# Performance work log

Hardware: AMD Instinct MI355X
Metric: run time of the kernel (lower is better)

## Reference

```python
import jax, jax.numpy as jnp
import numpy as np

B, N, E, T, DIN, H, G, ND, NT, L = 4, 10000, 320000, 16, 16, 64, 64, 16, 3, 7


def _mlp2(x, W1, b1, W2, b2):
    # Linear -> LeakyReLU -> (Dropout: eval identity) -> Linear -> LeakyReLU
    h = jax.nn.leaky_relu(x @ W1 + b1)
    return jax.nn.leaky_relu(h @ W2 + b2)


def _gcn_conv(x, src, dst, ew, nt, W1, b1, W2, b2):
    # x: [B,N,D], nt: [B,N,ND], ew: [*,E,1] broadcastable over batch
    x_in = _mlp2(jnp.concatenate([x, nt], axis=-1), W1, b1, W2, b2)  # [B,N,G]
    msgs = x_in[:, src, :] * ew                                      # gather + weight, [B,E,G]
    aggr = jnp.zeros(x_in.shape, x_in.dtype).at[:, dst, :].add(msgs) # scatter-add, [B,N,G]
    return x + aggr


def _gru(x, Wx, Wh, bx, bh):
    # PyTorch-style GRU over time axis. x: [B,N,T,DIN] -> hs: [T,B,N,H]
    xw = jnp.einsum('bntd,dh->tbnh', x, Wx) + bx  # precompute input projections [T,B,N,3H]
    h0 = jnp.zeros(x.shape[:2] + (Wh.shape[0],), x.dtype)

    def step(h, xw_t):
        hw = h @ Wh + bh
        xr, xz, xn = jnp.split(xw_t, 3, axis=-1)
        hr, hz, hn = jnp.split(hw, 3, axis=-1)
        r = jax.nn.sigmoid(xr + hr)
        z = jax.nn.sigmoid(xz + hz)
        n = jnp.tanh(xn + r * hn)
        h_new = (1 - z) * n + z * h
        return h_new, h_new

    _, hs = jax.lax.scan(step, h0, xw)
    return hs


def reference(input_day, edge_attr, gru_Wx, gru_Wh, gru_bx, gru_bh,
              rnn_fc_W, rnn_fc_b,
              e_emb, e_c0_W1, e_c0_b1, e_c0_W2, e_c0_b2,
              e_c1_W1, e_c1_b1, e_c1_W2, e_c1_b2,
              e_fm_W1, e_fm_b1, e_fm_W2, e_fm_b2,
              g_emb, g_c0_W1, g_c0_b1, g_c0_W2, g_c0_b2,
              g_c1_W1, g_c1_b1, g_c1_W2, g_c1_b2,
              gcn_fc_W, gcn_fc_b,
              edge_index, node_type_ids):
    src, dst = edge_index[0], edge_index[1]

    # KRNN encoder (GRU) + max over time + FC head
    hs = _gru(input_day, gru_Wx, gru_Wh, gru_bx, gru_bh)  # [T,B,N,H]
    rnn_out = hs.max(axis=0)                              # kr_out.max(dim=-2) -> [B,N,H]
    y_rnn = rnn_out @ rnn_fc_W + rnn_fc_b                 # [B,N,L]

    # EdgeNet: GCN stack on static edge_attr, then per-edge pair MLP -> gate
    nt_e = jnp.broadcast_to(e_emb[node_type_ids][None], (B, N, ND))
    ew0 = edge_attr.reshape(1, E, 1)
    x = rnn_out
    x = _gcn_conv(x, src, dst, ew0, nt_e, e_c0_W1, e_c0_b1, e_c0_W2, e_c0_b2)
    x = _gcn_conv(x, src, dst, ew0, nt_e, e_c1_W1, e_c1_b1, e_c1_W2, e_c1_b2)
    edge_x = jnp.concatenate([x[:, src, :], x[:, dst, :]], axis=-1)  # [B,E,2G]
    h = jax.nn.leaky_relu(edge_x @ e_fm_W1 + e_fm_b1)
    edge_gate = jax.nn.relu(h @ e_fm_W2 + e_fm_b2)                   # [B,E,1]

    # Main GCNNet with learned edge gates
    nt_g = jnp.broadcast_to(g_emb[node_type_ids][None], (B, N, ND))
    x = rnn_out
    x = _gcn_conv(x, src, dst, edge_gate, nt_g, g_c0_W1, g_c0_b1, g_c0_W2, g_c0_b2)
    x = _gcn_conv(x, src, dst, edge_gate, nt_g, g_c1_W1, g_c1_b1, g_c1_W2, g_c1_b2)
    y_gcn = x @ gcn_fc_W + gcn_fc_b                                  # [B,N,L]

    return y_rnn + y_gcn


def setup_inputs() -> dict:
    key = jax.random.key(0)
    ks = iter(jax.random.split(key, 48))

    def nrm(shape, s=0.1):
        return jax.random.normal(next(ks), shape, jnp.float32) * s

    inp = {}
    inp['input_day'] = jax.random.normal(next(ks), (B, N, T, DIN), jnp.float32)
    inp['edge_index'] = jax.random.randint(next(ks), (2, E), 0, N)
    inp['node_type_ids'] = jax.random.randint(next(ks), (N,), 0, NT)
    inp['edge_attr'] = jax.random.uniform(next(ks), (E,), jnp.float32)

    inp['gru_Wx'] = nrm((DIN, 3 * H))
    inp['gru_Wh'] = nrm((H, 3 * H))
    inp['gru_bx'] = jnp.zeros((3 * H,), jnp.float32)
    inp['gru_bh'] = jnp.zeros((3 * H,), jnp.float32)
    inp['rnn_fc_W'] = nrm((H, L))
    inp['rnn_fc_b'] = jnp.zeros((L,), jnp.float32)

    inp['e_emb'] = nrm((NT, ND))
    inp['g_emb'] = nrm((NT, ND))
    for pre, in_dim in (('e_c0', H + ND), ('e_c1', G + ND), ('g_c0', H + ND), ('g_c1', G + ND)):
        inp[pre + '_W1'] = nrm((in_dim, G))
        inp[pre + '_b1'] = jnp.zeros((G,), jnp.float32)
        inp[pre + '_W2'] = nrm((G, G))
        inp[pre + '_b2'] = jnp.zeros((G,), jnp.float32)

    inp['e_fm_W1'] = nrm((2 * G, G))
    inp['e_fm_b1'] = jnp.zeros((G,), jnp.float32)
    inp['e_fm_W2'] = nrm((G, 1))
    inp['e_fm_b2'] = jnp.zeros((1,), jnp.float32)

    inp['gcn_fc_W'] = nrm((G, L))
    inp['gcn_fc_b'] = jnp.zeros((L,), jnp.float32)
    return inp
```

## Files before the change

### kernel.cpp

```cpp
#include <hip/hip_runtime.h>
#include <hip/hip_bf16.h>

#define NB 4
#define NN 10000
#define NE 320000
#define BN 40000
#define NL 7

typedef float f32x4 __attribute__((ext_vector_type(4)));
typedef __bf16 bf16x8 __attribute__((ext_vector_type(8)));

__device__ __forceinline__ float bf2f(unsigned short u){
  unsigned x = ((unsigned)u) << 16;
  return __builtin_bit_cast(float, x);
}
__device__ __forceinline__ unsigned short f2bf(float f){
  unsigned u = __builtin_bit_cast(unsigned, f);
  u += 0x7fffu + ((u >> 16) & 1u);
  return (unsigned short)(u >> 16);
}
__device__ __forceinline__ __bf16 f2b(float f){
  return __builtin_bit_cast(__bf16, f2bf(f));
}
__device__ __forceinline__ bf16x8 zero8(){
  uint4 z = make_uint4(0u,0u,0u,0u);
  return __builtin_bit_cast(bf16x8, z);
}
__device__ __forceinline__ bf16x8 ld8bf(const unsigned short* p){
  uint4 u = *(const uint4*)p;
  return __builtin_bit_cast(bf16x8, u);
}
__device__ __forceinline__ bf16x8 ld8f(const float* p){
  float4 a = *(const float4*)p;
  float4 b = *(const float4*)(p+4);
  bf16x8 r;
  r[0]=f2b(a.x); r[1]=f2b(a.y); r[2]=f2b(a.z); r[3]=f2b(a.w);
  r[4]=f2b(b.x); r[5]=f2b(b.y); r[6]=f2b(b.z); r[7]=f2b(b.w);
  return r;
}
__device__ __forceinline__ float frcp(float x){ return __builtin_amdgcn_rcpf(x); }
__device__ __forceinline__ float sigm(float x){ return frcp(1.f+__expf(-x)); }
__device__ __forceinline__ float tanh_(float x){ return 1.f - 2.f*frcp(__expf(2.f*x)+1.f); }
__device__ __forceinline__ float lrelu(float x){ return x > 0.f ? x : 0.01f*x; }

#define LDS_WAIT() asm volatile("s_waitcnt lgkmcnt(0)" ::: "memory")

__global__ __launch_bounds__(256, 2) void gru_kernel(
    const float* __restrict__ xd,
    const float* __restrict__ Wx,
    const float* __restrict__ Wh,
    const float* __restrict__ bx,
    const float* __restrict__ bh,
    float* __restrict__ rnn)
{
  __shared__ __attribute__((aligned(16))) unsigned short WhT[192][72];
  __shared__ __attribute__((aligned(16))) unsigned short WxT[192][40];
  __shared__ __attribute__((aligned(16))) unsigned short hb[4][16][72];
  int tid = threadIdx.x;
  int wave = tid >> 6, lane = tid & 63;
  int ln16 = lane & 15, quad = lane >> 4;

  for (int i = tid; i < 64*192; i += 256){
    int k = i / 192, n = i - k*192;
    WhT[n][k] = f2bf(Wh[i]);
  }
  for (int i = tid; i < 16*192; i += 256){
    int k = i / 192, n = i - k*192;
    WxT[n][k] = f2bf(Wx[i]);
    WxT[n][16+k] = 0;
  }
  for (int i = tid; i < 4*16*72; i += 256) ((unsigned short*)hb)[i] = 0;
  __syncthreads();

  int rowbase = blockIdx.x * 64 + wave * 16;

  bf16x8 whf[2][12];
  #pragma unroll
  for (int kt=0; kt<2; ++kt)
    #pragma unroll
    for (int nt=0; nt<12; ++nt)
      whf[kt][nt] = ld8bf(&WhT[nt*16 + ln16][kt*32 + quad*8]);

  float br_[4], bz_[4], bxn_[4], bhn_[4];
  #pragma unroll
  for (int j=0;j<4;++j){
    br_[j]  = bx[j*16+ln16]     + bh[j*16+ln16];
    bz_[j]  = bx[(4+j)*16+ln16] + bh[(4+j)*16+ln16];
    bxn_[j] = bx[(8+j)*16+ln16];
    bhn_[j] = bh[(8+j)*16+ln16];
  }

  f32x4 hprev[4], vmax[4];
  #pragma unroll
  for (int j=0;j<4;++j){
    hprev[j] = (f32x4){0.f,0.f,0.f,0.f};
    vmax[j]  = (f32x4){-1e30f,-1e30f,-1e30f,-1e30f};
  }

  const float* xrow = xd + (size_t)(rowbase + ln16) * 256;
  unsigned short* hrow = &hb[wave][ln16][0];

  bf16x8 axc = (quad < 2) ? ld8f(xrow + quad*8) : zero8();

  for (int t = 0; t < 16; ++t){
    bf16x8 axn = (t < 15 && quad < 2) ? ld8f(xrow + (t+1)*16 + quad*8) : zero8();
    bf16x8 ah0 = ld8bf(hrow + quad*8);
    bf16x8 ah1 = ld8bf(hrow + 32 + quad*8);

    #pragma unroll
    for (int j=0;j<4;++j){
      bf16x8 xr = ld8bf(&WxT[j*16+ln16][quad*8]);
      bf16x8 xz = ld8bf(&WxT[(4+j)*16+ln16][quad*8]);
      bf16x8 xn = ld8bf(&WxT[(8+j)*16+ln16][quad*8]);
      f32x4 ar = (f32x4){br_[j],br_[j],br_[j],br_[j]};
      ar = __builtin_amdgcn_mfma_f32_16x16x32_bf16(axc, xr, ar, 0,0,0);
      ar = __builtin_amdgcn_mfma_f32_16x16x32_bf16(ah0, whf[0][j], ar, 0,0,0);
      ar = __builtin_amdgcn_mfma_f32_16x16x32_bf16(ah1, whf[1][j], ar, 0,0,0);
      f32x4 az = (f32x4){bz_[j],bz_[j],bz_[j],bz_[j]};
      az = __builtin_amdgcn_mfma_f32_16x16x32_bf16(axc, xz, az, 0,0,0);
      az = __builtin_amdgcn_mfma_f32_16x16x32_bf16(ah0, whf[0][4+j], az, 0,0,0);
      az = __builtin_amdgcn_mfma_f32_16x16x32_bf16(ah1, whf[1][4+j], az, 0,0,0);
      f32x4 an = (f32x4){bxn_[j],bxn_[j],bxn_[j],bxn_[j]};
      an = __builtin_amdgcn_mfma_f32_16x16x32_bf16(axc, xn, an, 0,0,0);
      f32x4 ah = (f32x4){bhn_[j],bhn_[j],bhn_[j],bhn_[j]};
      ah = __builtin_amdgcn_mfma_f32_16x16x32_bf16(ah0, whf[0][8+j], ah, 0,0,0);
      ah = __builtin_amdgcn_mfma_f32_16x16x32_bf16(ah1, whf[1][8+j], ah, 0,0,0);
      #pragma unroll
      for (int i=0;i<4;++i){
        float r  = sigm(ar[i]);
        float z  = sigm(az[i]);
        float nn = tanh_(an[i] + r * ah[i]);
        float h  = fmaf(z, hprev[j][i]-nn, nn);
        hprev[j][i] = h;
        vmax[j][i] = fmaxf(vmax[j][i], h);
        hb[wave][quad*4+i][j*16+ln16] = f2bf(h);
      }
    }
    LDS_WAIT();
    axc = axn;
  }
  #pragma unroll
  for (int j=0;j<4;++j)
    #pragma unroll
    for (int i=0;i<4;++i)
      rnn[(size_t)(rowbase + quad*4 + i)*64 + j*16 + ln16] = vmax[j][i];
}

__global__ __launch_bounds__(256, 2) void mlp2_kernel(
    const float* __restrict__ x,
    const int* __restrict__ ntid,
    const float* __restrict__ emb,
    const float* __restrict__ W1,
    const float* __restrict__ b1,
    const float* __restrict__ W2,
    const float* __restrict__ b2,
    unsigned short* __restrict__ out)
{
  __shared__ __attribute__((aligned(16))) unsigned short W1T[64][96];
  __shared__ __attribute__((aligned(16))) unsigned short W2T[64][72];
  __shared__ __attribute__((aligned(16))) unsigned short hb[4][16][72];
  __shared__ float sb1[64], sb2[64];
  int tid = threadIdx.x;
  for (int i=tid;i<80*64;i+=256){ int k=i>>6, n=i&63; W1T[n][k]=f2bf(W1[i]); }
  for (int i=tid;i<64*16;i+=256){ int n=i>>4, k=80+(i&15); W1T[n][k]=0; }
  for (int i=tid;i<64*64;i+=256){ int k=i>>6, n=i&63; W2T[n][k]=f2bf(W2[i]); }
  if (tid<64){ sb1[tid]=b1[tid]; sb2[tid]=b2[tid]; }
  __syncthreads();

  int wave = tid>>6, lane = tid&63, ln16 = lane&15, quad = lane>>4;
  int row0 = blockIdx.x*64 + wave*16;
  int r_ = row0 + ln16;
  const float* xr = x + (size_t)r_*64;
  bf16x8 a0 = ld8f(xr + quad*8);
  bf16x8 a1 = ld8f(xr + 32 + quad*8);
  int id = ntid[r_ % NN];
  bf16x8 a2 = (quad<2) ? ld8f(emb + id*16 + quad*8) : zero8();

  f32x4 acc[4];
  #pragma unroll
  for (int nt=0;nt<4;++nt){
    float bb = sb1[nt*16+ln16];
    acc[nt] = (f32x4){bb,bb,bb,bb};
    acc[nt] = __builtin_amdgcn_mfma_f32_16x16x32_bf16(a0, ld8bf(&W1T[nt*16+ln16][quad*8]),    acc[nt], 0,0,0);
    acc[nt] = __builtin_amdgcn_mfma_f32_16x16x32_bf16(a1, ld8bf(&W1T[nt*16+ln16][32+quad*8]), acc[nt], 0,0,0);
    acc[nt] = __builtin_amdgcn_mfma_f32_16x16x32_bf16(a2, ld8bf(&W1T[nt*16+ln16][64+quad*8]), acc[nt], 0,0,0);
  }
  #pragma unroll
  for (int nt=0;nt<4;++nt)
    #pragma unroll
    for (int i=0;i<4;++i)
      hb[wave][quad*4+i][nt*16+ln16] = f2bf(lrelu(acc[nt][i]));
  LDS_WAIT();
  bf16x8 h0 = ld8bf(&hb[wave][ln16][quad*8]);
  bf16x8 h1 = ld8bf(&hb[wave][ln16][32+quad*8]);
  f32x4 acc2[4];
  #pragma unroll
  for (int nt=0;nt<4;++nt){
    float bb = sb2[nt*16+ln16];
    acc2[nt] = (f32x4){bb,bb,bb,bb};
    acc2[nt] = __builtin_amdgcn_mfma_f32_16x16x32_bf16(h0, ld8bf(&W2T[nt*16+ln16][quad*8]),    acc2[nt], 0,0,0);
    acc2[nt] = __builtin_amdgcn_mfma_f32_16x16x32_bf16(h1, ld8bf(&W2T[nt*16+ln16][32+quad*8]), acc2[nt], 0,0,0);
  }
  #pragma unroll
  for (int nt=0;nt<4;++nt)
    #pragma unroll
    for (int i=0;i<4;++i)
      out[(size_t)(row0+quad*4+i)*64 + nt*16+ln16] = f2bf(lrelu(acc2[nt][i]));
}

__global__ __launch_bounds__(256, 2) void uv_kernel(
    const float* __restrict__ x,
    const float* __restrict__ W1,
    unsigned short* __restrict__ uvp)
{
  __shared__ __attribute__((aligned(16))) unsigned short WT[128][72];
  int tid=threadIdx.x;
  for (int i=tid;i<64*64;i+=256){
    int k=i>>6, n=i&63;
    WT[n][k]    = f2bf(W1[i]);
    WT[64+n][k] = f2bf(W1[64*64 + i]);
  }
  __syncthreads();
  int wave=tid>>6, lane=tid&63, ln16=lane&15, quad=lane>>4;
  int row0 = blockIdx.x*64 + wave*16;
  const float* xr = x + (size_t)(row0+ln16)*64;
  bf16x8 a0 = ld8f(xr + quad*8);
  bf16x8 a1 = ld8f(xr + 32 + quad*8);
  f32x4 acc[8];
  #pragma unroll
  for (int nt=0;nt<8;++nt){
    acc[nt] = (f32x4){0.f,0.f,0.f,0.f};
    acc[nt] = __builtin_amdgcn_mfma_f32_16x16x32_bf16(a0, ld8bf(&WT[nt*16+ln16][quad*8]),    acc[nt], 0,0,0);
    acc[nt] = __builtin_amdgcn_mfma_f32_16x16x32_bf16(a1, ld8bf(&WT[nt*16+ln16][32+quad*8]), acc[nt], 0,0,0);
  }
  #pragma unroll
  for (int nt=0;nt<8;++nt)
    #pragma unroll
    for (int i=0;i<4;++i)
      uvp[(size_t)(row0+quad*4+i)*128 + nt*16+ln16] = f2bf(acc[nt][i]);
}

__global__ __launch_bounds__(256) void count_kernel(const int* __restrict__ ei, int* __restrict__ counts){
  int e = blockIdx.x*256+threadIdx.x;
  atomicAdd(&counts[ei[NE+e]], 1);
}
__global__ __launch_bounds__(1024) void scan_kernel(const int* __restrict__ counts,
                                                    int* __restrict__ rowptr, int* __restrict__ cursor){
  __shared__ int incl[10240];
  __shared__ int wsum[16];
  int tid=threadIdx.x, wave=tid>>6, lane=tid&63;
  int base = wave*640;
  int carry=0;
  #pragma unroll
  for (int c=0;c<10;++c){
    int i = base + c*64 + lane;
    int v = (i<NN)? counts[i] : 0;
    int s = v;
    #pragma unroll
    for (int off=1;off<64;off<<=1){
      int t_ = __shfl_up(s, off);
      if (lane>=off) s += t_;
    }
    s += carry;
    incl[base + c*64 + lane] = s;
    carry = __shfl(s, 63);
  }
  if (lane==63) wsum[wave]=carry;
  __syncthreads();
  if (wave==0){
    int w_ = (lane<16)? wsum[lane]:0;
    #pragma unroll
    for (int off=1;off<16;off<<=1){
      int t_ = __shfl_up(w_, off);
      if (lane>=off) w_ += t_;
    }
    if (lane<16) wsum[lane]=w_;
  }
  __syncthreads();
  int woff = (wave>0)? wsum[wave-1] : 0;
  #pragma unroll
  for (int c=0;c<10;++c){
    int i = base + c*64 + lane;
    if (i<NN){
      int excl = incl[i] + woff - counts[i];
      rowptr[i]=excl; cursor[i]=excl;
    }
  }
  if (tid==0) rowptr[NN]=wsum[15];
}
__global__ __launch_bounds__(256) void fill_kernel(const int* __restrict__ ei,
                                                   const float* __restrict__ ea,
                                                   int* __restrict__ cursor,
                                                   int* __restrict__ ssrc,
                                                   float* __restrict__ wcsr){
  int e = blockIdx.x*256+threadIdx.x;
  int d = ei[NE+e];
  int pos = atomicAdd(&cursor[d],1);
  ssrc[pos]=ei[e];
  wcsr[pos]=ea[e];
}

__global__ __launch_bounds__(256) void aggr_kernel(
    const float* x,
    const unsigned short* __restrict__ xin,
    const int* __restrict__ rowptr,
    const int* __restrict__ ssrc,
    const float* __restrict__ wp,
    int bstride,
    float* out)
{
  int tid=threadIdx.x;
  int wave=tid>>6, lane=tid&63;
  int sub=lane>>4, l=lane&15;
  int bid = blockIdx.x*4 + wave;
  int b = bid / NN, n = bid - b*NN;
  int p0 = rowptr[n], p1 = rowptr[n+1];
  const unsigned short* xb_ = xin + (size_t)b*NN*64;
  const float* wb = wp + (size_t)b*bstride;
  float a0=0.f, a1=0.f, a2=0.f, a3=0.f;
  #pragma unroll 4
  for (int p=p0+sub; p<p1; p+=4){
    int s = ssrc[p];
    float w = wb[p];
    uint2 m = *(const uint2*)(xb_ + (size_t)s*64 + l*4);
    a0 += bf2f((unsigned short)(m.x & 0xffffu)) * w;
    a1 += bf2f((unsigned short)(m.x >> 16)) * w;
    a2 += bf2f((unsigned short)(m.y & 0xffffu)) * w;
    a3 += bf2f((unsigned short)(m.y >> 16)) * w;
  }
  a0 += __shfl_xor(a0,16); a0 += __shfl_xor(a0,32);
  a1 += __shfl_xor(a1,16); a1 += __shfl_xor(a1,32);
  a2 += __shfl_xor(a2,16); a2 += __shfl_xor(a2,32);
  a3 += __shfl_xor(a3,16); a3 += __shfl_xor(a3,32);
  if (sub==0){
    float4 base = *(const float4*)(x + (size_t)bid*64 + l*4);
    float4 o; o.x=base.x+a0; o.y=base.y+a1; o.z=base.z+a2; o.w=base.w+a3;
    *(float4*)(out + (size_t)bid*64 + l*4) = o;
  }
}

__global__ __launch_bounds__(256) void aggr_final_kernel(
    const float* x,
    const unsigned short* __restrict__ xin,
    const int* __restrict__ rowptr,
    const int* __restrict__ ssrc,
    const float* __restrict__ wp,
    const float* __restrict__ rnn,
    const float* __restrict__ Wr, const float* __restrict__ br,
    const float* __restrict__ Wg, const float* __restrict__ bg,
    float* __restrict__ out)
{
  __shared__ float sWr[448], sWg[448], sb[7];
  int tid=threadIdx.x;
  for (int i=tid;i<448;i+=256){ sWr[i]=Wr[i]; sWg[i]=Wg[i]; }
  if (tid<7) sb[tid]=br[tid]+bg[tid];
  __syncthreads();
  int wave=tid>>6, lane=tid&63;
  int sub=lane>>4, l=lane&15;
  int bid = blockIdx.x*4 + wave;
  int b = bid / NN, n = bid - b*NN;
  int p0 = rowptr[n], p1 = rowptr[n+1];
  const unsigned short* xb_ = xin + (size_t)b*NN*64;
  const float* wb = wp + (size_t)b*NE;
  float a0=0.f, a1=0.f, a2=0.f, a3=0.f;
  #pragma unroll 4
  for (int p=p0+sub; p<p1; p+=4){
    int s = ssrc[p];
    float w = wb[p];
    uint2 m = *(const uint2*)(xb_ + (size_t)s*64 + l*4);
    a0 += bf2f((unsigned short)(m.x & 0xffffu)) * w;
    a1 += bf2f((unsigned short)(m.x >> 16)) * w;
    a2 += bf2f((unsigned short)(m.y & 0xffffu)) * w;
    a3 += bf2f((unsigned short)(m.y >> 16)) * w;
  }
  a0 += __shfl_xor(a0,16); a0 += __shfl_xor(a0,32);
  a1 += __shfl_xor(a1,16); a1 += __shfl_xor(a1,32);
  a2 += __shfl_xor(a2,16); a2 += __shfl_xor(a2,32);
  a3 += __shfl_xor(a3,16); a3 += __shfl_xor(a3,32);
  if (sub==0){
    float4 base = *(const float4*)(x + (size_t)bid*64 + l*4);
    float o0=base.x+a0, o1=base.y+a1, o2=base.z+a2, o3=base.w+a3;
    float4 rr = *(const float4*)(rnn + (size_t)bid*64 + l*4);
    float part[7];
    #pragma unroll
    for (int q=0;q<7;++q)
      part[q] = o0*sWg[(l*4+0)*7+q] + o1*sWg[(l*4+1)*7+q]
              + o2*sWg[(l*4+2)*7+q] + o3*sWg[(l*4+3)*7+q]
              + rr.x*sWr[(l*4+0)*7+q] + rr.y*sWr[(l*4+1)*7+q]
              + rr.z*sWr[(l*4+2)*7+q] + rr.w*sWr[(l*4+3)*7+q];
    #pragma unroll
    for (int q=0;q<7;++q){
      part[q] += __shfl_xor(part[q],1);
      part[q] += __shfl_xor(part[q],2);
      part[q] += __shfl_xor(part[q],4);
      part[q] += __shfl_xor(part[q],8);
    }
    if (l==0){
      #pragma unroll
      for (int q=0;q<7;++q) out[(size_t)bid*7+q] = part[q] + sb[q];
    }
  }
}

__global__ __launch_bounds__(256) void gate_kernel(
    const unsigned short* __restrict__ uvp,
    const int* __restrict__ rowptr,
    const int* __restrict__ ssrc,
    const float* __restrict__ b1,
    const float* __restrict__ W2,
    const float* __restrict__ b2,
    float* __restrict__ gate)
{
  int tid=threadIdx.x;
  int wave=tid>>6, lane=tid&63;
  int sub=lane>>4, l=lane&15;
  int bid = blockIdx.x*4 + wave;
  int b = bid / NN, n = bid - b*NN;
  int p0 = rowptr[n], p1 = rowptr[n+1];
  const unsigned short* ub = uvp + (size_t)b*NN*128;
  uint2 vu = *(const uint2*)(ub + (size_t)n*128 + 64 + l*4);
  float v0=bf2f((unsigned short)(vu.x&0xffffu)), v1=bf2f((unsigned short)(vu.x>>16));
  float v2=bf2f((unsigned short)(vu.y&0xffffu)), v3=bf2f((unsigned short)(vu.y>>16));
  float4 bb = *(const float4*)(b1 + l*4);
  float4 ww = *(const float4*)(W2 + l*4);
  float b2v = b2[0];
  float* gb = gate + (size_t)b*NE;
  #pragma unroll 4
  for (int p=p0+sub; p<p1; p+=4){
    int s = ssrc[p];
    uint2 uu = *(const uint2*)(ub + (size_t)s*128 + l*4);
    float h0 = lrelu(bf2f((unsigned short)(uu.x&0xffffu)) + v0 + bb.x);
    float h1 = lrelu(bf2f((unsigned short)(uu.x>>16))     + v1 + bb.y);
    float h2 = lrelu(bf2f((unsigned short)(uu.y&0xffffu)) + v2 + bb.z);
    float h3 = lrelu(bf2f((unsigned short)(uu.y>>16))     + v3 + bb.w);
    float part = h0*ww.x + h1*ww.y + h2*ww.z + h3*ww.w;
    part += __shfl_xor(part,1);
    part += __shfl_xor(part,2);
    part += __shfl_xor(part,4);
    part += __shfl_xor(part,8);
    if (l==0){
      float g = part + b2v;
      gb[p] = g>0.f ? g : 0.f;
    }
  }
}

extern "C" void kernel_launch(void* const* d_in, const int* in_sizes, int n_in,
                              void* d_out, int out_size, void* d_ws, size_t ws_size,
                              hipStream_t stream)
{
  (void)in_sizes; (void)n_in; (void)out_size; (void)ws_size;
  const float* input_day = (const float*)d_in[0];
  const int* ei    = (const int*)d_in[1];
  const int* ntid  = (const int*)d_in[2];
  const float* edge_attr = (const float*)d_in[3];
  const float* gWx = (const float*)d_in[4];
  const float* gWh = (const float*)d_in[5];
  const float* gbx = (const float*)d_in[6];
  const float* gbh = (const float*)d_in[7];
  const float* rW  = (const float*)d_in[8];
  const float* rb  = (const float*)d_in[9];
  const float* eemb= (const float*)d_in[10];
  const float* gemb= (const float*)d_in[11];
  const float* ec0W1=(const float*)d_in[12];
  const float* ec0b1=(const float*)d_in[13];
  const float* ec0W2=(const float*)d_in[14];
  const float* ec0b2=(const float*)d_in[15];
  const float* ec1W1=(const float*)d_in[16];
  const float* ec1b1=(const float*)d_in[17];
  const float* ec1W2=(const float*)d_in[18];
  const float* ec1b2=(const float*)d_in[19];
  const float* gc0W1=(const float*)d_in[20];
  const float* gc0b1=(const float*)d_in[21];
  const float* gc0W2=(const float*)d_in[22];
  const float* gc0b2=(const float*)d_in[23];
  const float* gc1W1=(const float*)d_in[24];
  const float* gc1b1=(const float*)d_in[25];
  const float* gc1W2=(const float*)d_in[26];
  const float* gc1b2=(const float*)d_in[27];
  const float* efmW1=(const float*)d_in[28];
  const float* efmb1=(const float*)d_in[29];
  const float* efmW2=(const float*)d_in[30];
  const float* efmb2=(const float*)d_in[31];
  const float* gcnW =(const float*)d_in[32];
  const float* gcnb =(const float*)d_in[33];

  char* ws = (char*)d_ws;
  float*          rnn = (float*)(ws);
  float*          xe  = (float*)(ws + 10240000);
  unsigned short* xin = (unsigned short*)(ws + 20480000);
  unsigned short* uvp = (unsigned short*)(ws + 25600000);
  float*          gat = (float*)(ws + 35840000);
  int* rowptr= (int*)(ws + 40960000);
  int* cursor= (int*)(ws + 41000064);
  int* counts= (int*)(ws + 41040064);
  int*   ssrc= (int*)(ws + 41080064);
  float* wcsr= (float*)(ws + 42360064);

  hipMemsetAsync(counts, 0, NN*sizeof(int), stream);
  count_kernel<<<NE/256, 256, 0, stream>>>(ei, counts);
  scan_kernel<<<1, 1024, 0, stream>>>(counts, rowptr, cursor);
  fill_kernel<<<NE/256, 256, 0, stream>>>(ei, edge_attr, cursor, ssrc, wcsr);

  gru_kernel<<<625, 256, 0, stream>>>(input_day, gWx, gWh, gbx, gbh, rnn);

  mlp2_kernel<<<625, 256, 0, stream>>>(rnn, ntid, eemb, ec0W1, ec0b1, ec0W2, ec0b2, xin);
  aggr_kernel<<<BN/4, 256, 0, stream>>>(rnn, xin, rowptr, ssrc, wcsr, 0, xe);
  mlp2_kernel<<<625, 256, 0, stream>>>(xe, ntid, eemb, ec1W1, ec1b1, ec1W2, ec1b2, xin);
  aggr_kernel<<<BN/4, 256, 0, stream>>>(xe, xin, rowptr, ssrc, wcsr, 0, xe);

  uv_kernel<<<625, 256, 0, stream>>>(xe, efmW1, uvp);
  gate_kernel<<<BN/4, 256, 0, stream>>>(uvp, rowptr, ssrc, efmb1, efmW2, efmb2, gat);

  mlp2_kernel<<<625, 256, 0, stream>>>(rnn, ntid, gemb, gc0W1, gc0b1, gc0W2, gc0b2, xin);
  aggr_kernel<<<BN/4, 256, 0, stream>>>(rnn, xin, rowptr, ssrc, gat, NE, xe);
  mlp2_kernel<<<625, 256, 0, stream>>>(xe, ntid, gemb, gc1W1, gc1b1, gc1W2, gc1b2, xin);
  aggr_final_kernel<<<BN/4, 256, 0, stream>>>(xe, xin, rowptr, ssrc, gat, rnn,
                                              rW, rb, gcnW, gcnb, (float*)d_out);
}
```

Before: 470.1 us.

## Transpose GRU MFMA operands, fold biases into the matmul, pack bf16 stores

```diff
diff --git a/kernel.cpp b/kernel.cpp
--- a/kernel.cpp
+++ b/kernel.cpp
@@ -26,17 +26,24 @@
   uint4 z = make_uint4(0u,0u,0u,0u);
   return __builtin_bit_cast(bf16x8, z);
 }
+__device__ __forceinline__ bf16x8 one8(){
+  uint4 z = make_uint4(0x3f80u,0u,0u,0u);
+  return __builtin_bit_cast(bf16x8, z);
+}
 __device__ __forceinline__ bf16x8 ld8bf(const unsigned short* p){
   uint4 u = *(const uint4*)p;
   return __builtin_bit_cast(bf16x8, u);
 }
+__device__ __forceinline__ unsigned pk2(float lo, float hi){
+  unsigned r;
+  asm("v_cvt_pk_bf16_f32 %0, %1, %2" : "=v"(r) : "v"(lo), "v"(hi));
+  return r;
+}
 __device__ __forceinline__ bf16x8 ld8f(const float* p){
   float4 a = *(const float4*)p;
   float4 b = *(const float4*)(p+4);
-  bf16x8 r;
-  r[0]=f2b(a.x); r[1]=f2b(a.y); r[2]=f2b(a.z); r[3]=f2b(a.w);
-  r[4]=f2b(b.x); r[5]=f2b(b.y); r[6]=f2b(b.z); r[7]=f2b(b.w);
-  return r;
+  uint4 u = make_uint4(pk2(a.x,a.y), pk2(a.z,a.w), pk2(b.x,b.y), pk2(b.z,b.w));
+  return __builtin_bit_cast(bf16x8, u);
 }
 __device__ __forceinline__ float frcp(float x){ return __builtin_amdgcn_rcpf(x); }
 __device__ __forceinline__ float sigm(float x){ return frcp(1.f+__expf(-x)); }
@@ -67,7 +74,11 @@
   for (int i = tid; i < 16*192; i += 256){
     int k = i / 192, n = i - k*192;
     WxT[n][k] = f2bf(Wx[i]);
-    WxT[n][16+k] = 0;
+    WxT[n][17+k] = 0;
+  }
+  if (tid < 192){
+    float bias = (tid < 128) ? (bx[tid] + bh[tid]) : bx[tid];
+    WxT[tid][16] = f2bf(bias);
   }
   for (int i = tid; i < 4*16*72; i += 256) ((unsigned short*)hb)[i] = 0;
   __syncthreads();
@@ -81,14 +92,10 @@
     for (int nt=0; nt<12; ++nt)
       whf[kt][nt] = ld8bf(&WhT[nt*16 + ln16][kt*32 + quad*8]);
 
-  float br_[4], bz_[4], bxn_[4], bhn_[4];
-  #pragma unroll
-  for (int j=0;j<4;++j){
-    br_[j]  = bx[j*16+ln16]     + bh[j*16+ln16];
-    bz_[j]  = bx[(4+j)*16+ln16] + bh[(4+j)*16+ln16];
-    bxn_[j] = bx[(8+j)*16+ln16];
-    bhn_[j] = bh[(8+j)*16+ln16];
-  }
+  f32x4 bhn2[4];
+  #pragma unroll
+  for (int j=0;j<4;++j)
+    bhn2[j] = *(const f32x4*)(bh + 128 + j*16 + quad*4);
 
   f32x4 hprev[4], vmax[4];
   #pragma unroll
@@ -100,10 +107,14 @@
   const float* xrow = xd + (size_t)(rowbase + ln16) * 256;
   unsigned short* hrow = &hb[wave][ln16][0];
 
-  bf16x8 axc = (quad < 2) ? ld8f(xrow + quad*8) : zero8();
+  bf16x8 axc;
+  if (quad < 2) axc = ld8f(xrow + quad*8);
+  else          axc = (quad == 2) ? one8() : zero8();
 
   for (int t = 0; t < 16; ++t){
-    bf16x8 axn = (t < 15 && quad < 2) ? ld8f(xrow + (t+1)*16 + quad*8) : zero8();
+    bf16x8 axn;
+    if (quad < 2) axn = (t < 15) ? ld8f(xrow + (t+1)*16 + quad*8) : zero8();
+    else          axn = (quad == 2) ? one8() : zero8();
     bf16x8 ah0 = ld8bf(hrow + quad*8);
     bf16x8 ah1 = ld8bf(hrow + 32 + quad*8);
 
@@ -112,19 +123,17 @@
       bf16x8 xr = ld8bf(&WxT[j*16+ln16][quad*8]);
       bf16x8 xz = ld8bf(&WxT[(4+j)*16+ln16][quad*8]);
       bf16x8 xn = ld8bf(&WxT[(8+j)*16+ln16][quad*8]);
-      f32x4 ar = (f32x4){br_[j],br_[j],br_[j],br_[j]};
-      ar = __builtin_amdgcn_mfma_f32_16x16x32_bf16(axc, xr, ar, 0,0,0);
-      ar = __builtin_amdgcn_mfma_f32_16x16x32_bf16(ah0, whf[0][j], ar, 0,0,0);
-      ar = __builtin_amdgcn_mfma_f32_16x16x32_bf16(ah1, whf[1][j], ar, 0,0,0);
-      f32x4 az = (f32x4){bz_[j],bz_[j],bz_[j],bz_[j]};
-      az = __builtin_amdgcn_mfma_f32_16x16x32_bf16(axc, xz, az, 0,0,0);
-      az = __builtin_amdgcn_mfma_f32_16x16x32_bf16(ah0, whf[0][4+j], az, 0,0,0);
-      az = __builtin_amdgcn_mfma_f32_16x16x32_bf16(ah1, whf[1][4+j], az, 0,0,0);
-      f32x4 an = (f32x4){bxn_[j],bxn_[j],bxn_[j],bxn_[j]};
-      an = __builtin_amdgcn_mfma_f32_16x16x32_bf16(axc, xn, an, 0,0,0);
-      f32x4 ah = (f32x4){bhn_[j],bhn_[j],bhn_[j],bhn_[j]};
-      ah = __builtin_amdgcn_mfma_f32_16x16x32_bf16(ah0, whf[0][8+j], ah, 0,0,0);
-      ah = __builtin_amdgcn_mfma_f32_16x16x32_bf16(ah1, whf[1][8+j], ah, 0,0,0);
+      f32x4 z4 = (f32x4){0.f,0.f,0.f,0.f};
+      f32x4 ar = __builtin_amdgcn_mfma_f32_16x16x32_bf16(xr, axc, z4, 0,0,0);
+      ar = __builtin_amdgcn_mfma_f32_16x16x32_bf16(whf[0][j], ah0, ar, 0,0,0);
+      ar = __builtin_amdgcn_mfma_f32_16x16x32_bf16(whf[1][j], ah1, ar, 0,0,0);
+      f32x4 az = __builtin_amdgcn_mfma_f32_16x16x32_bf16(xz, axc, z4, 0,0,0);
+      az = __builtin_amdgcn_mfma_f32_16x16x32_bf16(whf[0][4+j], ah0, az, 0,0,0);
+      az = __builtin_amdgcn_mfma_f32_16x16x32_bf16(whf[1][4+j], ah1, az, 0,0,0);
+      f32x4 an = __builtin_amdgcn_mfma_f32_16x16x32_bf16(xn, axc, z4, 0,0,0);
+      f32x4 ah = __builtin_amdgcn_mfma_f32_16x16x32_bf16(whf[0][8+j], ah0, bhn2[j], 0,0,0);
+      ah = __builtin_amdgcn_mfma_f32_16x16x32_bf16(whf[1][8+j], ah1, ah, 0,0,0);
+      f32x4 hv;
       #pragma unroll
       for (int i=0;i<4;++i){
         float r  = sigm(ar[i]);
@@ -133,17 +142,17 @@
         float h  = fmaf(z, hprev[j][i]-nn, nn);
         hprev[j][i] = h;
         vmax[j][i] = fmaxf(vmax[j][i], h);
-        hb[wave][quad*4+i][j*16+ln16] = f2bf(h);
+        hv[i] = h;
       }
+      *(uint2*)&hb[wave][ln16][j*16+quad*4] = make_uint2(pk2(hv[0],hv[1]), pk2(hv[2],hv[3]));
     }
     LDS_WAIT();
     axc = axn;
   }
+  float* orow = rnn + (size_t)(rowbase + ln16)*64;
   #pragma unroll
   for (int j=0;j<4;++j)
-    #pragma unroll
-    for (int i=0;i<4;++i)
-      rnn[(size_t)(rowbase + quad*4 + i)*64 + j*16 + ln16] = vmax[j][i];
+    *(f32x4*)(orow + j*16 + quad*4) = vmax[j];
 }
 
 __global__ __launch_bounds__(256, 2) void mlp2_kernel(
```

New measurement: 462.0 us. No clear change (-1.7%).
